# Kernel optimization log

Measured on AMD Instinct MI355X. Metric: run time of the kernel, lower is better.

Reference implementation:

```python
import jax, jax.numpy as jnp
import numpy as np

NEG_SLOPE = 0.2  # PyG GATConv default leaky_relu negative_slope
BN_EPS = 1e-5


def gat_layer(x, src, dst, W, a_src, a_dst, bias):
    """PyG-style GATConv (self-loops already appended to src/dst).
    x: [N, F_in], W: [F_in, H*C], a_src/a_dst: [H, C], bias: [H*C].
    Returns [N, H*C] (concat heads)."""
    N = x.shape[0]
    H, C = a_src.shape
    h = (x @ W).reshape(N, H, C)                      # [N, H, C]
    al_src = jnp.sum(h * a_src[None], axis=-1)        # [N, H]
    al_dst = jnp.sum(h * a_dst[None], axis=-1)        # [N, H]
    e = jax.nn.leaky_relu(al_src[src] + al_dst[dst], NEG_SLOPE)  # [E, H]
    # segment softmax over destination neighborhoods
    m = jax.ops.segment_max(e, dst, num_segments=N)   # [N, H]
    ee = jnp.exp(e - m[dst])
    denom = jax.ops.segment_sum(ee, dst, num_segments=N)  # [N, H]
    alpha = ee / denom[dst]                           # [E, H]
    out = jax.ops.segment_sum(alpha[:, :, None] * h[src], dst, num_segments=N)  # [N, H, C]
    return out.reshape(N, H * C) + bias


def batch_norm(x, gamma, beta):
    mu = jnp.mean(x, axis=0)
    var = jnp.var(x, axis=0)  # biased, matches torch BN training stats
    return gamma * (x - mu) * jax.lax.rsqrt(var + BN_EPS) + beta


def setup_inputs() -> dict:
    key = jax.random.key(0)
    N, F, H, C = 50000, 128, 4, 64
    E = 400000
    HC = H * C  # 256
    ks = jax.random.split(key, 24)

    def glorot(k, shape, fan_in):
        return jax.random.normal(k, shape, dtype=jnp.float32) * (1.0 / np.sqrt(fan_in))

    inp = {
        "x": jax.random.normal(ks[0], (N, F), dtype=jnp.float32),
        "edge_index": jax.random.randint(ks[1], (2, E), 0, N, dtype=jnp.int64),
        # conv1: F -> H*C
        "W1": glorot(ks[2], (F, HC), F),
        "a1s": glorot(ks[3], (H, C), C),
        "a1d": glorot(ks[4], (H, C), C),
        "b1": jnp.zeros((HC,), jnp.float32),
        # conv2: H*C -> H*C
        "W2": glorot(ks[5], (HC, HC), HC),
        "a2s": glorot(ks[6], (H, C), C),
        "a2d": glorot(ks[7], (H, C), C),
        "b2": jnp.zeros((HC,), jnp.float32),
        # conv3: H*C -> C (1 head)
        "W3": glorot(ks[8], (HC, C), HC),
        "a3s": glorot(ks[9], (1, C), C),
        "a3d": glorot(ks[10], (1, C), C),
        "b3": jnp.zeros((C,), jnp.float32),
        # batch norms
        "g1": jnp.ones((HC,), jnp.float32),
        "be1": jnp.zeros((HC,), jnp.float32),
        "g2": jnp.ones((HC,), jnp.float32),
        "be2": jnp.zeros((HC,), jnp.float32),
        # MLP head: C -> C//2 -> 2
        "fw1": glorot(ks[11], (C, C // 2), C),
        "fb1": jnp.zeros((C // 2,), jnp.float32),
        "fw2": glorot(ks[12], (C // 2, 2), C // 2),
        "fb2": jnp.zeros((2,), jnp.float32),
    }
    return inp


def reference(x, edge_index, W1, a1s, a1d, b1, W2, a2s, a2d, b2,
              W3, a3s, a3d, b3, g1, be1, g2, be2, fw1, fb1, fw2, fb2):
    N = x.shape[0]
    loop = jnp.arange(N, dtype=edge_index.dtype)
    src = jnp.concatenate([edge_index[0], loop])  # self-loops (PyG default)
    dst = jnp.concatenate([edge_index[1], loop])

    h = gat_layer(x, src, dst, W1, a1s, a1d, b1)
    h = jax.nn.elu(batch_norm(h, g1, be1))
    h = gat_layer(h, src, dst, W2, a2s, a2d, b2)
    h = jax.nn.elu(batch_norm(h, g2, be2))
    h = jax.nn.elu(gat_layer(h, src, dst, W3, a3s, a3d, b3))
    h = jax.nn.relu(h @ fw1 + fb1)
    return h @ fw2 + fb2  # [N, 2] logits
```

## Files before the change

### kernel.cpp

```cpp
#include <hip/hip_runtime.h>
#include <math.h>
#include <stdint.h>

typedef __attribute__((ext_vector_type(8))) short short8v;
typedef __attribute__((ext_vector_type(4))) float float4v;

__device__ __forceinline__ float bf2f(unsigned short u) {
  return __uint_as_float((unsigned int)u << 16);
}
__device__ __forceinline__ unsigned short f2bf(float f) {
  unsigned int u = __float_as_uint(f);
  unsigned int r = (u + 0x7FFFu + ((u >> 16) & 1u)) >> 16;
  return (unsigned short)r;
}
__device__ __forceinline__ float exp_lrelu(float x) {
  x = x > 0.f ? x : 0.2f * x;
  return expf(x);
}

typedef __attribute__((address_space(3))) void lds_void;
typedef const __attribute__((address_space(1))) void glb_void;
__device__ __forceinline__ void gload_lds16(const void* g, void* l) {
  __builtin_amdgcn_global_load_lds((glb_void*)g, (lds_void*)l, 16, 0, 0);
}

__device__ __forceinline__ void wprep_one(const float* W, unsigned short* Wh,
                                          int t, int K, int Nw)
{
  int i = t & 7;
  int lane = (t >> 3) & 63;
  int frag = t >> 9;
  int ktiles = K >> 5;
  int n_tile = frag / ktiles, k_tile = frag - n_tile * ktiles;
  int k = k_tile * 32 + ((lane >> 4) << 3) + i;
  int n = (n_tile << 4) + (lane & 15);
  Wh[t] = f2bf(W[(size_t)k * Nw + n]);
}

__global__ void wprep_all_kernel(const float* __restrict__ W1, unsigned short* __restrict__ w1h,
                                 const float* __restrict__ W2, unsigned short* __restrict__ w2h,
                                 const float* __restrict__ W3, unsigned short* __restrict__ w3h)
{
  int t = blockIdx.x * 256 + threadIdx.x;
  const int s1 = 128 * 256, s2 = 256 * 256, s3 = 256 * 64;
  if (t < s1) { wprep_one(W1, w1h, t, 128, 256); return; }
  t -= s1;
  if (t < s2) { wprep_one(W2, w2h, t, 256, 256); return; }
  t -= s2;
  if (t < s3) { wprep_one(W3, w3h, t, 256, 64); }
}

__global__ __launch_bounds__(256) void split_kernel(const float* __restrict__ in,
    unsigned short* __restrict__ hi, size_t n4)
{
  size_t i0 = (size_t)blockIdx.x * 256 + threadIdx.x;
  size_t stride = (size_t)gridDim.x * 256;
  for (size_t idx = i0; idx < n4; idx += stride) {
    float4 v = ((const float4*)in)[idx];
    ushort4 h;
    h.x = f2bf(v.x); h.y = f2bf(v.y); h.z = f2bf(v.z); h.w = f2bf(v.w);
    ((ushort4*)hi)[idx] = h;
  }
}

__global__ __launch_bounds__(256) void bnsplit_kernel(const unsigned short* __restrict__ act,
    const float* __restrict__ scale, const float* __restrict__ shift,
    unsigned short* __restrict__ hi, size_t nchunks)
{
  size_t i0 = (size_t)blockIdx.x * 256 + threadIdx.x;
  size_t stride = (size_t)gridDim.x * 256;
  for (size_t idx = i0; idx < nchunks; idx += stride) {
    ushort4 u = ((const ushort4*)act)[idx];
    int f = (int)((idx * 4) & 255);
    float4 sc = *(const float4*)(scale + f);
    float4 sh = *(const float4*)(shift + f);
    float v0 = fmaf(bf2f(u.x), sc.x, sh.x);
    float v1 = fmaf(bf2f(u.y), sc.y, sh.y);
    float v2 = fmaf(bf2f(u.z), sc.z, sh.z);
    float v3 = fmaf(bf2f(u.w), sc.w, sh.w);
    v0 = v0 > 0.f ? v0 : expm1f(v0);
    v1 = v1 > 0.f ? v1 : expm1f(v1);
    v2 = v2 > 0.f ? v2 : expm1f(v2);
    v3 = v3 > 0.f ? v3 : expm1f(v3);
    ushort4 h;
    h.x = f2bf(v0); h.y = f2bf(v1); h.z = f2bf(v2); h.w = f2bf(v3);
    ((ushort4*)hi)[idx] = h;
  }
}

template<int MI, int WM, int WN, int KSTEPS, int HEADS>
__global__ __launch_bounds__(128) void gemm_al(
    const unsigned short* __restrict__ Ah, const unsigned short* __restrict__ Bh,
    const float* __restrict__ a_s, const float* __restrict__ a_d,
    unsigned short* __restrict__ C, float* __restrict__ al_s, float* __restrict__ al_d,
    int M)
{
  constexpr int NWAVES = WM * WN;
  constexpr int BM = WM * MI * 16;
  constexpr int TILEB = BM * 64 * 2;
  constexpr int Nw = HEADS * 64;
  constexpr int K = KSTEPS * 64;
  constexpr int KT32 = KSTEPS * 2;
  __shared__ __align__(16) unsigned char smem[2][TILEB];

  const int wid = threadIdx.x >> 6, lane = threadIdx.x & 63;
  const int wm = wid / WN, wn = wid % WN;
  const int gn = blockIdx.y * WN + wn;
  const int m0 = blockIdx.x * BM;
  const int n0 = gn * 64;
  const int ar = lane & 15;
  const int cchunk = lane >> 4;
  const int ntile0 = n0 >> 4;

  float4v acc[MI][4];
#pragma unroll
  for (int mi = 0; mi < MI; ++mi)
#pragma unroll
    for (int ni = 0; ni < 4; ++ni)
      acc[mi][ni] = (float4v){0.f, 0.f, 0.f, 0.f};

  auto stage = [&](int buf, int ks) {
#pragma unroll
    for (int c = wid; c < 8; c += NWAVES) {
      const unsigned short* gp = Ah + (size_t)(m0 + lane) * K + ks * 64 + c * 8;
      gload_lds16(gp, &smem[buf][c * 1024 + lane * 16]);
    }
  };

  stage(0, 0);
  int cur = 0;
  for (int ks = 0; ks < KSTEPS; ++ks) {
    __syncthreads();
    short8v bh[2][4];
#pragma unroll
    for (int hh = 0; hh < 2; ++hh)
#pragma unroll
      for (int ni = 0; ni < 4; ++ni) {
        int kt = ks * 2 + hh;
        size_t off = (((size_t)(ntile0 + ni) * KT32 + kt) * 64 + lane) * 8;
        bh[hh][ni] = *(const short8v*)(Bh + off);
      }
    if (ks + 1 < KSTEPS) stage(cur ^ 1, ks + 1);
    short8v ah[2][MI];
#pragma unroll
    for (int hh = 0; hh < 2; ++hh)
#pragma unroll
      for (int mi = 0; mi < MI; ++mi) {
        int row = wm * MI * 16 + mi * 16 + ar;
        int c = hh * 4 + cchunk;
        int off = c * 1024 + row * 16;
        ah[hh][mi] = *(const short8v*)&smem[cur][off];
      }
#pragma unroll
    for (int hh = 0; hh < 2; ++hh)
#pragma unroll
      for (int mi = 0; mi < MI; ++mi)
#pragma unroll
        for (int ni = 0; ni < 4; ++ni)
          acc[mi][ni] = __builtin_amdgcn_mfma_f32_16x16x32_bf16(ah[hh][mi], bh[hh][ni], acc[mi][ni], 0, 0, 0);
    cur ^= 1;
  }

  const int cc = lane & 15;
#pragma unroll
  for (int mi = 0; mi < MI; ++mi) {
    int rowb = m0 + wm * MI * 16 + mi * 16 + ((lane >> 4) << 2);
#pragma unroll
    for (int r = 0; r < 4; ++r) {
      int row = rowb + r;
      if (row < M) {
#pragma unroll
        for (int ni = 0; ni < 4; ++ni)
          C[(size_t)row * Nw + n0 + ni * 16 + cc] = f2bf(acc[mi][ni][r]);
      }
    }
  }

  const int head = (HEADS == 4) ? gn : 0;
  float as_[4], ad_[4];
#pragma unroll
  for (int ni = 0; ni < 4; ++ni) {
    as_[ni] = a_s[head * 64 + ni * 16 + cc];
    ad_[ni] = a_d[head * 64 + ni * 16 + cc];
  }
#pragma unroll
  for (int mi = 0; mi < MI; ++mi) {
#pragma unroll
    for (int r = 0; r < 4; ++r) {
      float h0 = bf2f(f2bf(acc[mi][0][r]));
      float h1 = bf2f(f2bf(acc[mi][1][r]));
      float h2 = bf2f(f2bf(acc[mi][2][r]));
      float h3 = bf2f(f2bf(acc[mi][3][r]));
      float ps = h0 * as_[0] + h1 * as_[1] + h2 * as_[2] + h3 * as_[3];
      float pd = h0 * ad_[0] + h1 * ad_[1] + h2 * ad_[2] + h3 * ad_[3];
#pragma unroll
      for (int off = 1; off < 16; off <<= 1) {
        ps += __shfl_xor(ps, off);
        pd += __shfl_xor(pd, off);
      }
      int row = m0 + wm * MI * 16 + mi * 16 + ((lane >> 4) << 2) + r;
      if (cc == 0 && row < M) {
        al_s[row * HEADS + head] = ps;
        al_d[row * HEADS + head] = pd;
      }
    }
  }
}

__global__ void count_kernel(const int* __restrict__ dst, int E, int Etot, int* __restrict__ counts)
{
  int e = blockIdx.x * 256 + threadIdx.x;
  if (e >= Etot) return;
  int d = (e < E) ? dst[e] : (e - E);
  atomicAdd(&counts[d], 1);
}

__global__ void block_sum_kernel(const int* __restrict__ counts, int N, int* __restrict__ bsums)
{
  __shared__ int sd[256];
  int i = blockIdx.x * 256 + threadIdx.x;
  sd[threadIdx.x] = (i < N) ? counts[i] : 0;
  __syncthreads();
  for (int off = 128; off; off >>= 1) {
    if (threadIdx.x < off) sd[threadIdx.x] += sd[threadIdx.x + off];
    __syncthreads();
  }
  if (threadIdx.x == 0) bsums[blockIdx.x] = sd[0];
}

__global__ void scan_bsums_kernel(int* bsums, int nb)
{
  __shared__ int sd[256];
  int t = threadIdx.x;
  int v = (t < nb) ? bsums[t] : 0;
  sd[t] = v;
  __syncthreads();
  for (int off = 1; off < 256; off <<= 1) {
    int x = (t >= off) ? sd[t - off] : 0;
    __syncthreads();
    sd[t] += x;
    __syncthreads();
  }
  if (t < nb) bsums[t] = sd[t] - v;
}

__global__ void scan_write_kernel(const int* __restrict__ counts, int N,
                                  const int* __restrict__ bsums, int* __restrict__ rowStart, int Etot)
{
  __shared__ int sd[256];
  int i = blockIdx.x * 256 + threadIdx.x;
  int v = (i < N) ? counts[i] : 0;
  sd[threadIdx.x] = v;
  __syncthreads();
  for (int off = 1; off < 256; off <<= 1) {
    int x = (threadIdx.x >= off) ? sd[threadIdx.x - off] : 0;
    __syncthreads();
    sd[threadIdx.x] += x;
    __syncthreads();
  }
  if (i < N) rowStart[i] = bsums[blockIdx.x] + sd[threadIdx.x] - v;
  if (i == N - 1) rowStart[N] = Etot;
}

__global__ void fill_kernel(const int* __restrict__ src, const int* __restrict__ dst,
                            int E, int Etot, const int* __restrict__ rowStart,
                            int* __restrict__ cursor, int* __restrict__ csrSrc)
{
  int e = blockIdx.x * 256 + threadIdx.x;
  if (e >= Etot) return;
  int s, d;
  if (e < E) { s = src[e]; d = dst[e]; } else { s = d = e - E; }
  int pos = rowStart[d] + atomicAdd(&cursor[d], 1);
  csrSrc[pos] = s;
}

template<int HC_, bool OUT16>
__global__ __launch_bounds__(256) void aggregate_fused(
    const unsigned short* __restrict__ h16,
    const float* __restrict__ als, const float* __restrict__ ald,
    const int* __restrict__ csrSrc, const int* __restrict__ rowStart,
    void* __restrict__ outp, int N, const float* __restrict__ bias, int doElu)
{
  constexpr int H_ = HC_ / 64;
  constexpr int FPL = HC_ / 64;
  __shared__ float ldsW[4][64 * H_];
  const int wl = threadIdx.x >> 6;
  int wid = blockIdx.x * 4 + wl;
  if (wid >= N) return;
  const int lane = threadIdx.x & 63;
  const int head = (H_ == 4) ? (lane >> 4) : 0;
  const int start = rowStart[wid], end = rowStart[wid + 1];

  float ad0, ad1, ad2, ad3;
  if (H_ == 4) {
    float4 adv = ((const float4*)ald)[wid];
    ad0 = adv.x; ad1 = adv.y; ad2 = adv.z; ad3 = adv.w;
  } else {
    ad0 = ald[wid]; ad1 = ad2 = ad3 = 0.f;
  }

  float acc[FPL] = {};
  float wsum = 0.f;

  for (int base = start; base < end; base += 64) {
    int cnt = end - base; if (cnt > 64) cnt = 64;
    int s_l = 0;
    if (lane < cnt) {
      s_l = csrSrc[base + lane];
      if (H_ == 4) {
        float4 av = ((const float4*)als)[s_l];
        float4 w4;
        w4.x = exp_lrelu(av.x + ad0);
        w4.y = exp_lrelu(av.y + ad1);
        w4.z = exp_lrelu(av.z + ad2);
        w4.w = exp_lrelu(av.w + ad3);
        *(float4*)&ldsW[wl][lane * 4] = w4;
      } else {
        ldsW[wl][lane] = exp_lrelu(als[s_l] + ad0);
      }
    }
    int i = 0;
    for (; i + 4 <= cnt; i += 4) {
      int s0 = __shfl(s_l, i);
      int s1 = __shfl(s_l, i + 1);
      int s2 = __shfl(s_l, i + 2);
      int s3 = __shfl(s_l, i + 3);
      float w0 = ldsW[wl][(i + 0) * H_ + head];
      float w1 = ldsW[wl][(i + 1) * H_ + head];
      float w2 = ldsW[wl][(i + 2) * H_ + head];
      float w3 = ldsW[wl][(i + 3) * H_ + head];
      if (FPL == 4) {
        ushort4 r0 = ((const ushort4*)(h16 + (size_t)s0 * HC_))[lane];
        ushort4 r1 = ((const ushort4*)(h16 + (size_t)s1 * HC_))[lane];
        ushort4 r2 = ((const ushort4*)(h16 + (size_t)s2 * HC_))[lane];
        ushort4 r3 = ((const ushort4*)(h16 + (size_t)s3 * HC_))[lane];
        wsum += (w0 + w1) + (w2 + w3);
        acc[0] = fmaf(w0, bf2f(r0.x), acc[0]);
        acc[1] = fmaf(w0, bf2f(r0.y), acc[1]);
        acc[2] = fmaf(w0, bf2f(r0.z), acc[2]);
        acc[3] = fmaf(w0, bf2f(r0.w), acc[3]);
        acc[0] = fmaf(w1, bf2f(r1.x), acc[0]);
        acc[1] = fmaf(w1, bf2f(r1.y), acc[1]);
        acc[2] = fmaf(w1, bf2f(r1.z), acc[2]);
        acc[3] = fmaf(w1, bf2f(r1.w), acc[3]);
        acc[0] = fmaf(w2, bf2f(r2.x), acc[0]);
        acc[1] = fmaf(w2, bf2f(r2.y), acc[1]);
        acc[2] = fmaf(w2, bf2f(r2.z), acc[2]);
        acc[3] = fmaf(w2, bf2f(r2.w), acc[3]);
        acc[0] = fmaf(w3, bf2f(r3.x), acc[0]);
        acc[1] = fmaf(w3, bf2f(r3.y), acc[1]);
        acc[2] = fmaf(w3, bf2f(r3.z), acc[2]);
        acc[3] = fmaf(w3, bf2f(r3.w), acc[3]);
      } else {
        unsigned short r0 = h16[(size_t)s0 * HC_ + lane];
        unsigned short r1 = h16[(size_t)s1 * HC_ + lane];
        unsigned short r2 = h16[(size_t)s2 * HC_ + lane];
        unsigned short r3 = h16[(size_t)s3 * HC_ + lane];
        wsum += (w0 + w1) + (w2 + w3);
        acc[0] = fmaf(w0, bf2f(r0), acc[0]);
        acc[0] = fmaf(w1, bf2f(r1), acc[0]);
        acc[0] = fmaf(w2, bf2f(r2), acc[0]);
        acc[0] = fmaf(w3, bf2f(r3), acc[0]);
      }
    }
    for (; i < cnt; ++i) {
      int s0 = __shfl(s_l, i);
      float w0 = ldsW[wl][i * H_ + head];
      wsum += w0;
      if (FPL == 4) {
        ushort4 r0 = ((const ushort4*)(h16 + (size_t)s0 * HC_))[lane];
        acc[0] = fmaf(w0, bf2f(r0.x), acc[0]);
        acc[1] = fmaf(w0, bf2f(r0.y), acc[1]);
        acc[2] = fmaf(w0, bf2f(r0.z), acc[2]);
        acc[3] = fmaf(w0, bf2f(r0.w), acc[3]);
      } else {
        unsigned short r0 = h16[(size_t)s0 * HC_ + lane];
        acc[0] = fmaf(w0, bf2f(r0), acc[0]);
      }
    }
  }

  float inv = 1.0f / wsum;
  if (FPL == 4) {
    float o0 = acc[0] * inv, o1 = acc[1] * inv, o2 = acc[2] * inv, o3 = acc[3] * inv;
    if (bias) {
      const float4 b = ((const float4*)bias)[lane];
      o0 += b.x; o1 += b.y; o2 += b.z; o3 += b.w;
    }
    if (doElu) {
      o0 = o0 > 0.f ? o0 : expm1f(o0);
      o1 = o1 > 0.f ? o1 : expm1f(o1);
      o2 = o2 > 0.f ? o2 : expm1f(o2);
      o3 = o3 > 0.f ? o3 : expm1f(o3);
    }
    if (OUT16) {
      ushort4 o;
      o.x = f2bf(o0); o.y = f2bf(o1); o.z = f2bf(o2); o.w = f2bf(o3);
      ((ushort4*)((unsigned short*)outp + (size_t)wid * HC_))[lane] = o;
    } else {
      ((float4*)((float*)outp + (size_t)wid * HC_))[lane] = make_float4(o0, o1, o2, o3);
    }
  } else {
    float o = acc[0] * inv;
    if (bias) o += bias[lane];
    if (doElu) o = o > 0.f ? o : expm1f(o);
    if (OUT16) ((unsigned short*)outp)[(size_t)wid * HC_ + lane] = f2bf(o);
    else       ((float*)outp)[(size_t)wid * HC_ + lane] = o;
  }
}

__global__ __launch_bounds__(256) void bn_stats_kernel(const unsigned short* __restrict__ x, int N,
                                float* __restrict__ partials)
{
  const int wid = threadIdx.x >> 6, lane = threadIdx.x & 63;
  const int gw = blockIdx.x * 4 + wid;
  const int tw = gridDim.x * 4;
  float4 s = make_float4(0.f, 0.f, 0.f, 0.f);
  float4 q = make_float4(0.f, 0.f, 0.f, 0.f);
#pragma unroll 4
  for (int r = gw; r < N; r += tw) {
    ushort4 u = ((const ushort4*)(x + (size_t)r * 256))[lane];
    float v0 = bf2f(u.x), v1 = bf2f(u.y), v2 = bf2f(u.z), v3 = bf2f(u.w);
    s.x += v0; s.y += v1; s.z += v2; s.w += v3;
    q.x = fmaf(v0, v0, q.x); q.y = fmaf(v1, v1, q.y);
    q.z = fmaf(v2, v2, q.z); q.w = fmaf(v3, v3, q.w);
  }
  __shared__ float ls[4][512];
  *(float4*)&ls[wid][lane * 4] = s;
  *(float4*)&ls[wid][256 + lane * 4] = q;
  __syncthreads();
  const int t = threadIdx.x;
  float a = ls[0][t] + ls[1][t] + ls[2][t] + ls[3][t];
  float b = ls[0][t + 256] + ls[1][t + 256] + ls[2][t + 256] + ls[3][t + 256];
  partials[blockIdx.x * 512 + t] = a;
  partials[blockIdx.x * 512 + 256 + t] = b;
}

__global__ void bn_final_kernel(const float* __restrict__ partials, int nblk,
                                const float* __restrict__ g, const float* __restrict__ be,
                                int N, float* __restrict__ scale, float* __restrict__ shift)
{
  int f = threadIdx.x;
  float s = 0.f, q = 0.f;
#pragma unroll 8
  for (int b = 0; b < nblk; ++b) {
    s += partials[b * 512 + f];
    q += partials[b * 512 + 256 + f];
  }
  float mu = s / N;
  float var = q / N - mu * mu;
  float rs = rsqrtf(var + 1e-5f);
  float sc = g[f] * rs;
  scale[f] = sc;
  shift[f] = be[f] - mu * sc;
}

__global__ __launch_bounds__(256) void mlp_kernel(const float* __restrict__ h,
                           const float* __restrict__ fw1,
                           const float* __restrict__ fb1, const float* __restrict__ fw2,
                           const float* __restrict__ fb2, float* __restrict__ out, int N)
{
  __shared__ float w1s[64][32];
  __shared__ float w2s[32][2];
  __shared__ float b1s[32];
  const int t = threadIdx.x;
  for (int i = t; i < 64 * 32; i += 256) w1s[i >> 5][i & 31] = fw1[i];
  if (t < 64) w2s[t >> 1][t & 1] = fw2[t];
  if (t < 32) b1s[t] = fb1[t];
  __syncthreads();

  int n = blockIdx.x * 256 + t;
  if (n >= N) return;

  float hv[64];
#pragma unroll
  for (int k4 = 0; k4 < 16; ++k4) {
    float4 v = *(const float4*)(h + (size_t)n * 64 + k4 * 4);
    hv[k4 * 4 + 0] = v.x; hv[k4 * 4 + 1] = v.y;
    hv[k4 * 4 + 2] = v.z; hv[k4 * 4 + 3] = v.w;
  }
  float hid[32];
#pragma unroll
  for (int j = 0; j < 32; ++j) hid[j] = b1s[j];
#pragma unroll
  for (int k = 0; k < 64; ++k) {
    float hk = hv[k];
#pragma unroll
    for (int jb = 0; jb < 8; ++jb) {
      float4 wv = *(const float4*)&w1s[k][jb * 4];
      hid[jb * 4 + 0] = fmaf(hk, wv.x, hid[jb * 4 + 0]);
      hid[jb * 4 + 1] = fmaf(hk, wv.y, hid[jb * 4 + 1]);
      hid[jb * 4 + 2] = fmaf(hk, wv.z, hid[jb * 4 + 2]);
      hid[jb * 4 + 3] = fmaf(hk, wv.w, hid[jb * 4 + 3]);
    }
  }
  float p0 = fb2[0], p1 = fb2[1];
#pragma unroll
  for (int j = 0; j < 32; ++j) {
    float r = fmaxf(hid[j], 0.f);
    p0 = fmaf(r, w2s[j][0], p0);
    p1 = fmaf(r, w2s[j][1], p1);
  }
  *(float2*)(out + (size_t)n * 2) = make_float2(p0, p1);
}

extern "C" void kernel_launch(void* const* d_in, const int* in_sizes, int n_in,
                              void* d_out, int out_size, void* d_ws, size_t ws_size,
                              hipStream_t stream)
{
  const float* x   = (const float*)d_in[0];
  const int*   ei  = (const int*)d_in[1];
  const float* W1  = (const float*)d_in[2];
  const float* a1s = (const float*)d_in[3];
  const float* a1d = (const float*)d_in[4];
  const float* W2  = (const float*)d_in[6];
  const float* a2s = (const float*)d_in[7];
  const float* a2d = (const float*)d_in[8];
  const float* W3  = (const float*)d_in[10];
  const float* a3s = (const float*)d_in[11];
  const float* a3d = (const float*)d_in[12];
  const float* b3  = (const float*)d_in[13];
  const float* g1  = (const float*)d_in[14];
  const float* be1 = (const float*)d_in[15];
  const float* g2  = (const float*)d_in[16];
  const float* be2 = (const float*)d_in[17];
  const float* fw1 = (const float*)d_in[18];
  const float* fb1 = (const float*)d_in[19];
  const float* fw2 = (const float*)d_in[20];
  const float* fb2 = (const float*)d_in[21];
  float* out = (float*)d_out;

  const int F = 128;
  const int N = in_sizes[0] / F;
  const int E = in_sizes[1] / 2;
  const int Etot = E + N;
  const int* srcIdx = ei;
  const int* dstIdx = ei + E;

  char* w = (char*)d_ws;
  auto alloc = [&](size_t bytes) -> void* {
    void* p = (void*)w;
    w += (bytes + 255) & ~(size_t)255;
    return p;
  };
  unsigned short* h16  = (unsigned short*)alloc((size_t)N * 256 * 2);
  unsigned short* act16= (unsigned short*)alloc((size_t)N * 256 * 2);
  float* actf    = (float*)alloc((size_t)N * 64 * 4);
  unsigned short* aBf  = (unsigned short*)alloc((size_t)N * 256 * 2);
  float* als     = (float*)alloc((size_t)N * 4 * 4);
  float* ald     = (float*)alloc((size_t)N * 4 * 4);
  const size_t cntPad = ((size_t)N * 4 + 255) & ~(size_t)255;
  int*   counts  = (int*)alloc((size_t)N * 4);
  int*   cursor  = (int*)alloc((size_t)N * 4);
  int*   rowStart= (int*)alloc((size_t)(N + 1) * 4);
  int*   csrSrc  = (int*)alloc((size_t)Etot * 4);
  int*   bsums   = (int*)alloc((size_t)((N + 255) / 256) * 4);
  float* partials= (float*)alloc((size_t)128 * 512 * 4);
  float* scale1  = (float*)alloc(256 * 4);
  float* shift1  = (float*)alloc(256 * 4);
  float* scale2  = (float*)alloc(256 * 4);
  float* shift2  = (float*)alloc(256 * 4);
  unsigned short* w1h = (unsigned short*)alloc((size_t)128 * 256 * 2);
  unsigned short* w2h = (unsigned short*)alloc((size_t)256 * 256 * 2);
  unsigned short* w3h = (unsigned short*)alloc((size_t)256 * 64 * 2);
  (void)alloc(65536);

  const int nb = (N + 255) / 256;
  const int ebk = (Etot + 255) / 256;
  const int aggBlocks = (N + 3) / 4;

  const int wtot = 128 * 256 + 256 * 256 + 256 * 64;
  wprep_all_kernel<<<(wtot + 255) / 256, 256, 0, stream>>>(W1, w1h, W2, w2h, W3, w3h);

  hipMemsetAsync(counts, 0, cntPad + (size_t)N * 4, stream);
  count_kernel<<<ebk, 256, 0, stream>>>(dstIdx, E, Etot, counts);
  block_sum_kernel<<<nb, 256, 0, stream>>>(counts, N, bsums);
  scan_bsums_kernel<<<1, 256, 0, stream>>>(bsums, nb);
  scan_write_kernel<<<nb, 256, 0, stream>>>(counts, N, bsums, rowStart, Etot);
  fill_kernel<<<ebk, 256, 0, stream>>>(srcIdx, dstIdx, E, Etot, rowStart, cursor, csrSrc);

  dim3 g12((N + 63) / 64, 2);
  dim3 g3((N + 63) / 64, 1);

  split_kernel<<<2048, 256, 0, stream>>>(x, aBf, (size_t)N * 128 / 4);
  gemm_al<4, 1, 2, 2, 4><<<g12, 128, 0, stream>>>(aBf, w1h, a1s, a1d, h16, als, ald, N);
  aggregate_fused<256, true><<<aggBlocks, 256, 0, stream>>>(h16, als, ald, csrSrc, rowStart, act16, N, nullptr, 0);
  bn_stats_kernel<<<128, 256, 0, stream>>>(act16, N, partials);
  bn_final_kernel<<<1, 256, 0, stream>>>(partials, 128, g1, be1, N, scale1, shift1);

  bnsplit_kernel<<<2048, 256, 0, stream>>>(act16, scale1, shift1, aBf, (size_t)N * 64);
  gemm_al<4, 1, 2, 4, 4><<<g12, 128, 0, stream>>>(aBf, w2h, a2s, a2d, h16, als, ald, N);
  aggregate_fused<256, true><<<aggBlocks, 256, 0, stream>>>(h16, als, ald, csrSrc, rowStart, act16, N, nullptr, 0);
  bn_stats_kernel<<<128, 256, 0, stream>>>(act16, N, partials);
  bn_final_kernel<<<1, 256, 0, stream>>>(partials, 128, g2, be2, N, scale2, shift2);

  bnsplit_kernel<<<2048, 256, 0, stream>>>(act16, scale2, shift2, aBf, (size_t)N * 64);
  gemm_al<2, 2, 1, 4, 1><<<g3, 128, 0, stream>>>(aBf, w3h, a3s, a3d, h16, als, ald, N);
  aggregate_fused<64, false><<<aggBlocks, 256, 0, stream>>>(h16, als, ald, csrSrc, rowStart, actf, N, b3, 1);

  mlp_kernel<<<(N + 255) / 256, 256, 0, stream>>>(actf, fw1, fb1, fw2, fb2, out, N);
}
```

Measured before the change: 306.1 us.

## Fuse bf16 conversion and BN+ELU into GEMM A-loads, fuse MLP into last aggregation

Removes the standalone split and bnsplit kernels by loading the fp32 input or the bf16 activations directly in the GEMM, applying the BN scale/shift and ELU in registers, and writing the result to LDS. The global_load_lds staging is replaced by register loads followed by an LDS write after the MFMAs, which keeps double buffering. The layer-3 aggregation now also runs the MLP head per node, dropping the fp32 intermediate buffer and the separate mlp kernel. This saves several full-tensor memory round trips and launches. In exchange, the GEMM repeats the expm1 work for each N-tile block and does more VALU work and register traffic per tile.

```diff
diff --git a/kernel.cpp b/kernel.cpp
--- a/kernel.cpp
+++ b/kernel.cpp
@@ -16,12 +16,6 @@
 __device__ __forceinline__ float exp_lrelu(float x) {
   x = x > 0.f ? x : 0.2f * x;
   return expf(x);
-}
-
-typedef __attribute__((address_space(3))) void lds_void;
-typedef const __attribute__((address_space(1))) void glb_void;
-__device__ __forceinline__ void gload_lds16(const void* g, void* l) {
-  __builtin_amdgcn_global_load_lds((glb_void*)g, (lds_void*)l, 16, 0, 0);
 }
 
 __device__ __forceinline__ void wprep_one(const float* W, unsigned short* Wh,
@@ -50,60 +44,23 @@
   if (t < s3) { wprep_one(W3, w3h, t, 256, 64); }
 }
 
-__global__ __launch_bounds__(256) void split_kernel(const float* __restrict__ in,
-    unsigned short* __restrict__ hi, size_t n4)
-{
-  size_t i0 = (size_t)blockIdx.x * 256 + threadIdx.x;
-  size_t stride = (size_t)gridDim.x * 256;
-  for (size_t idx = i0; idx < n4; idx += stride) {
-    float4 v = ((const float4*)in)[idx];
-    ushort4 h;
-    h.x = f2bf(v.x); h.y = f2bf(v.y); h.z = f2bf(v.z); h.w = f2bf(v.w);
-    ((ushort4*)hi)[idx] = h;
-  }
-}
-
-__global__ __launch_bounds__(256) void bnsplit_kernel(const unsigned short* __restrict__ act,
+template<int MI, int WM, int WN, int KSTEPS, int HEADS, bool SRCF32>
+__global__ __launch_bounds__(128) void gemm_bn_al(
+    const void* __restrict__ AsrcV,
     const float* __restrict__ scale, const float* __restrict__ shift,
-    unsigned short* __restrict__ hi, size_t nchunks)
-{
-  size_t i0 = (size_t)blockIdx.x * 256 + threadIdx.x;
-  size_t stride = (size_t)gridDim.x * 256;
-  for (size_t idx = i0; idx < nchunks; idx += stride) {
-    ushort4 u = ((const ushort4*)act)[idx];
-    int f = (int)((idx * 4) & 255);
-    float4 sc = *(const float4*)(scale + f);
-    float4 sh = *(const float4*)(shift + f);
-    float v0 = fmaf(bf2f(u.x), sc.x, sh.x);
-    float v1 = fmaf(bf2f(u.y), sc.y, sh.y);
-    float v2 = fmaf(bf2f(u.z), sc.z, sh.z);
-    float v3 = fmaf(bf2f(u.w), sc.w, sh.w);
-    v0 = v0 > 0.f ? v0 : expm1f(v0);
-    v1 = v1 > 0.f ? v1 : expm1f(v1);
-    v2 = v2 > 0.f ? v2 : expm1f(v2);
-    v3 = v3 > 0.f ? v3 : expm1f(v3);
-    ushort4 h;
-    h.x = f2bf(v0); h.y = f2bf(v1); h.z = f2bf(v2); h.w = f2bf(v3);
-    ((ushort4*)hi)[idx] = h;
-  }
-}
-
-template<int MI, int WM, int WN, int KSTEPS, int HEADS>
-__global__ __launch_bounds__(128) void gemm_al(
-    const unsigned short* __restrict__ Ah, const unsigned short* __restrict__ Bh,
+    const unsigned short* __restrict__ Bh,
     const float* __restrict__ a_s, const float* __restrict__ a_d,
     unsigned short* __restrict__ C, float* __restrict__ al_s, float* __restrict__ al_d,
     int M)
 {
-  constexpr int NWAVES = WM * WN;
   constexpr int BM = WM * MI * 16;
-  constexpr int TILEB = BM * 64 * 2;
   constexpr int Nw = HEADS * 64;
   constexpr int K = KSTEPS * 64;
   constexpr int KT32 = KSTEPS * 2;
-  __shared__ __align__(16) unsigned char smem[2][TILEB];
-
-  const int wid = threadIdx.x >> 6, lane = threadIdx.x & 63;
+  __shared__ __align__(16) unsigned char smem[2][8192];
+
+  const int tid = threadIdx.x;
+  const int wid = tid >> 6, lane = tid & 63;
   const int wm = wid / WN, wn = wid % WN;
   const int gn = blockIdx.y * WN + wn;
   const int m0 = blockIdx.x * BM;
@@ -111,6 +68,7 @@
   const int ar = lane & 15;
   const int cchunk = lane >> 4;
   const int ntile0 = n0 >> 4;
+  const int srow = min(m0 + (tid & 63), M - 1);
 
   float4v acc[MI][4];
 #pragma unroll
@@ -119,15 +77,53 @@
     for (int ni = 0; ni < 4; ++ni)
       acc[mi][ni] = (float4v){0.f, 0.f, 0.f, 0.f};
 
-  auto stage = [&](int buf, int ks) {
-#pragma unroll
-    for (int c = wid; c < 8; c += NWAVES) {
-      const unsigned short* gp = Ah + (size_t)(m0 + lane) * K + ks * 64 + c * 8;
-      gload_lds16(gp, &smem[buf][c * 1024 + lane * 16]);
+  float4 rv0[4], rv1[4];
+  short8v ru[4];
+
+  auto LOADS = [&](int ks) {
+#pragma unroll
+    for (int j = 0; j < 4; ++j) {
+      int c = 2 * j + wid;
+      if constexpr (SRCF32) {
+        const float* p = (const float*)AsrcV + (size_t)srow * K + ks * 64 + c * 8;
+        rv0[j] = *(const float4*)p;
+        rv1[j] = *(const float4*)(p + 4);
+      } else {
+        const unsigned short* p = (const unsigned short*)AsrcV + (size_t)srow * K + ks * 64 + c * 8;
+        ru[j] = *(const short8v*)p;
+      }
     }
   };
-
-  stage(0, 0);
+  auto XWRITE = [&](int buf, int ks) {
+#pragma unroll
+    for (int j = 0; j < 4; ++j) {
+      int c = 2 * j + wid;
+      int r = tid & 63;
+      short8v wv;
+      if constexpr (SRCF32) {
+        float v[8] = {rv0[j].x, rv0[j].y, rv0[j].z, rv0[j].w,
+                      rv1[j].x, rv1[j].y, rv1[j].z, rv1[j].w};
+#pragma unroll
+        for (int i = 0; i < 8; ++i) wv[i] = (short)f2bf(v[i]);
+      } else {
+        int f = ks * 64 + c * 8;
+        float4 sc0 = *(const float4*)(scale + f), sc1 = *(const float4*)(scale + f + 4);
+        float4 sh0 = *(const float4*)(shift + f), sh1 = *(const float4*)(shift + f + 4);
+        float sc[8] = {sc0.x, sc0.y, sc0.z, sc0.w, sc1.x, sc1.y, sc1.z, sc1.w};
+        float sh[8] = {sh0.x, sh0.y, sh0.z, sh0.w, sh1.x, sh1.y, sh1.z, sh1.w};
+#pragma unroll
+        for (int i = 0; i < 8; ++i) {
+          float t = fmaf(bf2f((unsigned short)ru[j][i]), sc[i], sh[i]);
+          t = t > 0.f ? t : expm1f(t);
+          wv[i] = (short)f2bf(t);
+        }
+      }
+      *(short8v*)&smem[buf][c * 1024 + r * 16] = wv;
+    }
+  };
+
+  LOADS(0);
+  XWRITE(0, 0);
   int cur = 0;
   for (int ks = 0; ks < KSTEPS; ++ks) {
     __syncthreads();
@@ -140,7 +136,7 @@
         size_t off = (((size_t)(ntile0 + ni) * KT32 + kt) * 64 + lane) * 8;
         bh[hh][ni] = *(const short8v*)(Bh + off);
       }
-    if (ks + 1 < KSTEPS) stage(cur ^ 1, ks + 1);
+    if (ks + 1 < KSTEPS) LOADS(ks + 1);
     short8v ah[2][MI];
 #pragma unroll
     for (int hh = 0; hh < 2; ++hh)
@@ -148,8 +144,7 @@
       for (int mi = 0; mi < MI; ++mi) {
         int row = wm * MI * 16 + mi * 16 + ar;
         int c = hh * 4 + cchunk;
-        int off = c * 1024 + row * 16;
-        ah[hh][mi] = *(const short8v*)&smem[cur][off];
+        ah[hh][mi] = *(const short8v*)&smem[cur][c * 1024 + row * 16];
       }
 #pragma unroll
     for (int hh = 0; hh < 2; ++hh)
@@ -158,6 +153,7 @@
 #pragma unroll
         for (int ni = 0; ni < 4; ++ni)
           acc[mi][ni] = __builtin_amdgcn_mfma_f32_16x16x32_bf16(ah[hh][mi], bh[hh][ni], acc[mi][ni], 0, 0, 0);
+    if (ks + 1 < KSTEPS) XWRITE(cur ^ 1, ks + 1);
     cur ^= 1;
   }
 
@@ -274,32 +270,22 @@
   csrSrc[pos] = s;
 }
 
-template<int HC_, bool OUT16>
-__global__ __launch_bounds__(256) void aggregate_fused(
+__global__ __launch_bounds__(256) void aggregate_fused4(
     const unsigned short* __restrict__ h16,
     const float* __restrict__ als, const float* __restrict__ ald,
     const int* __restrict__ csrSrc, const int* __restrict__ rowStart,
-    void* __restrict__ outp, int N, const float* __restrict__ bias, int doElu)
-{
-  constexpr int H_ = HC_ / 64;
-  constexpr int FPL = HC_ / 64;
-  __shared__ float ldsW[4][64 * H_];
+    unsigned short* __restrict__ outp, int N)
+{
+  __shared__ float ldsW[4][256];
   const int wl = threadIdx.x >> 6;
   int wid = blockIdx.x * 4 + wl;
   if (wid >= N) return;
   const int lane = threadIdx.x & 63;
-  const int head = (H_ == 4) ? (lane >> 4) : 0;
+  const int head = lane >> 4;
   const int start = rowStart[wid], end = rowStart[wid + 1];
 
-  float ad0, ad1, ad2, ad3;
-  if (H_ == 4) {
-    float4 adv = ((const float4*)ald)[wid];
-    ad0 = adv.x; ad1 = adv.y; ad2 = adv.z; ad3 = adv.w;
-  } else {
-    ad0 = ald[wid]; ad1 = ad2 = ad3 = 0.f;
-  }
-
-  float acc[FPL] = {};
+  float4 adv = ((const float4*)ald)[wid];
+  float acc[4] = {};
   float wsum = 0.f;
 
   for (int base = start; base < end; base += 64) {
@@ -307,17 +293,13 @@
     int s_l = 0;
     if (lane < cnt) {
       s_l = csrSrc[base + lane];
-      if (H_ == 4) {
-        float4 av = ((const float4*)als)[s_l];
-        float4 w4;
-        w4.x = exp_lrelu(av.x + ad0);
-        w4.y = exp_lrelu(av.y + ad1);
-        w4.z = exp_lrelu(av.z + ad2);
-        w4.w = exp_lrelu(av.w + ad3);
-        *(float4*)&ldsW[wl][lane * 4] = w4;
-      } else {
-        ldsW[wl][lane] = exp_lrelu(als[s_l] + ad0);
-      }
+      float4 av = ((const float4*)als)[s_l];
+      float4 w4;
+      w4.x = exp_lrelu(av.x + adv.x);
+      w4.y = exp_lrelu(av.y + adv.y);
+      w4.z = exp_lrelu(av.z + adv.z);
+      w4.w = exp_lrelu(av.w + adv.w);
+      *(float4*)&ldsW[wl][lane * 4] = w4;
     }
     int i = 0;
     for (; i + 4 <= cnt; i += 4) {
@@ -325,88 +307,127 @@
       int s1 = __shfl(s_l, i + 1);
       int s2 = __shfl(s_l, i + 2);
       int s3 = __shfl(s_l, i + 3);
-      float w0 = ldsW[wl][(i + 0) * H_ + head];
-      float w1 = ldsW[wl][(i + 1) * H_ + head];
-      float w2 = ldsW[wl][(i + 2) * H_ + head];
-      float w3 = ldsW[wl][(i + 3) * H_ + head];
-      if (FPL == 4) {
-        ushort4 r0 = ((const ushort4*)(h16 + (size_t)s0 * HC_))[lane];
-        ushort4 r1 = ((const ushort4*)(h16 + (size_t)s1 * HC_))[lane];
-        ushort4 r2 = ((const ushort4*)(h16 + (size_t)s2 * HC_))[lane];
-        ushort4 r3 = ((const ushort4*)(h16 + (size_t)s3 * HC_))[lane];
-        wsum += (w0 + w1) + (w2 + w3);
-        acc[0] = fmaf(w0, bf2f(r0.x), acc[0]);
-        acc[1] = fmaf(w0, bf2f(r0.y), acc[1]);
-        acc[2] = fmaf(w0, bf2f(r0.z), acc[2]);
-        acc[3] = fmaf(w0, bf2f(r0.w), acc[3]);
-        acc[0] = fmaf(w1, bf2f(r1.x), acc[0]);
-        acc[1] = fmaf(w1, bf2f(r1.y), acc[1]);
-        acc[2] = fmaf(w1, bf2f(r1.z), acc[2]);
-        acc[3] = fmaf(w1, bf2f(r1.w), acc[3]);
-        acc[0] = fmaf(w2, bf2f(r2.x), acc[0]);
-        acc[1] = fmaf(w2, bf2f(r2.y), acc[1]);
-        acc[2] = fmaf(w2, bf2f(r2.z), acc[2]);
-        acc[3] = fmaf(w2, bf2f(r2.w), acc[3]);
-        acc[0] = fmaf(w3, bf2f(r3.x), acc[0]);
-        acc[1] = fmaf(w3, bf2f(r3.y), acc[1]);
-        acc[2] = fmaf(w3, bf2f(r3.z), acc[2]);
-        acc[3] = fmaf(w3, bf2f(r3.w), acc[3]);
-      } else {
-        unsigned short r0 = h16[(size_t)s0 * HC_ + lane];
-        unsigned short r1 = h16[(size_t)s1 * HC_ + lane];
-        unsigned short r2 = h16[(size_t)s2 * HC_ + lane];
-        unsigned short r3 = h16[(size_t)s3 * HC_ + lane];
-        wsum += (w0 + w1) + (w2 + w3);
-        acc[0] = fmaf(w0, bf2f(r0), acc[0]);
-        acc[0] = fmaf(w1, bf2f(r1), acc[0]);
-        acc[0] = fmaf(w2, bf2f(r2), acc[0]);
-        acc[0] = fmaf(w3, bf2f(r3), acc[0]);
-      }
+      float w0 = ldsW[wl][(i + 0) * 4 + head];
+      float w1 = ldsW[wl][(i + 1) * 4 + head];
+      float w2 = ldsW[wl][(i + 2) * 4 + head];
+      float w3 = ldsW[wl][(i + 3) * 4 + head];
+      ushort4 r0 = ((const ushort4*)(h16 + (size_t)s0 * 256))[lane];
+      ushort4 r1 = ((const ushort4*)(h16 + (size_t)s1 * 256))[lane];
+      ushort4 r2 = ((const ushort4*)(h16 + (size_t)s2 * 256))[lane];
+      ushort4 r3 = ((const ushort4*)(h16 + (size_t)s3 * 256))[lane];
+      wsum += (w0 + w1) + (w2 + w3);
+      acc[0] = fmaf(w0, bf2f(r0.x), acc[0]);
+      acc[1] = fmaf(w0, bf2f(r0.y), acc[1]);
+      acc[2] = fmaf(w0, bf2f(r0.z), acc[2]);
+      acc[3] = fmaf(w0, bf2f(r0.w), acc[3]);
+      acc[0] = fmaf(w1, bf2f(r1.x), acc[0]);
+      acc[1] = fmaf(w1, bf2f(r1.y), acc[1]);
+      acc[2] = fmaf(w1, bf2f(r1.z), acc[2]);
+      acc[3] = fmaf(w1, bf2f(r1.w), acc[3]);
+      acc[0] = fmaf(w2, bf2f(r2.x), acc[0]);
+      acc[1] = fmaf(w2, bf2f(r2.y), acc[1]);
+      acc[2] = fmaf(w2, bf2f(r2.z), acc[2]);
+      acc[3] = fmaf(w2, bf2f(r2.w), acc[3]);
+      acc[0] = fmaf(w3, bf2f(r3.x), acc[0]);
+      acc[1] = fmaf(w3, bf2f(r3.y), acc[1]);
+      acc[2] = fmaf(w3, bf2f(r3.z), acc[2]);
+      acc[3] = fmaf(w3, bf2f(r3.w), acc[3]);
     }
     for (; i < cnt; ++i) {
       int s0 = __shfl(s_l, i);
-      float w0 = ldsW[wl][i * H_ + head];
+      float w0 = ldsW[wl][i * 4 + head];
       wsum += w0;
-      if (FPL == 4) {
-        ushort4 r0 = ((const ushort4*)(h16 + (size_t)s0 * HC_))[lane];
-        acc[0] = fmaf(w0, bf2f(r0.x), acc[0]);
-        acc[1] = fmaf(w0, bf2f(r0.y), acc[1]);
-        acc[2] = fmaf(w0, bf2f(r0.z), acc[2]);
-        acc[3] = fmaf(w0, bf2f(r0.w), acc[3]);
-      } else {
-        unsigned short r0 = h16[(size_t)s0 * HC_ + lane];
-        acc[0] = fmaf(w0, bf2f(r0), acc[0]);
-      }
+      ushort4 r0 = ((const ushort4*)(h16 + (size_t)s0 * 256))[lane];
+      acc[0] = fmaf(w0, bf2f(r0.x), acc[0]);
+      acc[1] = fmaf(w0, bf2f(r0.y), acc[1]);
+      acc[2] = fmaf(w0, bf2f(r0.z), acc[2]);
+      acc[3] = fmaf(w0, bf2f(r0.w), acc[3]);
     }
   }
 
   float inv = 1.0f / wsum;
-  if (FPL == 4) {
-    float o0 = acc[0] * inv, o1 = acc[1] * inv, o2 = acc[2] * inv, o3 = acc[3] * inv;
-    if (bias) {
-      const float4 b = ((const float4*)bias)[lane];
-      o0 += b.x; o1 += b.y; o2 += b.z; o3 += b.w;
-    }
-    if (doElu) {
-      o0 = o0 > 0.f ? o0 : expm1f(o0);
-      o1 = o1 > 0.f ? o1 : expm1f(o1);
-      o2 = o2 > 0.f ? o2 : expm1f(o2);
-      o3 = o3 > 0.f ? o3 : expm1f(o3);
-    }
-    if (OUT16) {
-      ushort4 o;
-      o.x = f2bf(o0); o.y = f2bf(o1); o.z = f2bf(o2); o.w = f2bf(o3);
-      ((ushort4*)((unsigned short*)outp + (size_t)wid * HC_))[lane] = o;
-    } else {
-      ((float4*)((float*)outp + (size_t)wid * HC_))[lane] = make_float4(o0, o1, o2, o3);
-    }
-  } else {
-    float o = acc[0] * inv;
-    if (bias) o += bias[lane];
-    if (doElu) o = o > 0.f ? o : expm1f(o);
-    if (OUT16) ((unsigned short*)outp)[(size_t)wid * HC_ + lane] = f2bf(o);
-    else       ((float*)outp)[(size_t)wid * HC_ + lane] = o;
-  }
+  ushort4 o;
+  o.x = f2bf(acc[0] * inv); o.y = f2bf(acc[1] * inv);
+  o.z = f2bf(acc[2] * inv); o.w = f2bf(acc[3] * inv);
+  ((ushort4*)(outp + (size_t)wid * 256))[lane] = o;
+}
+
+__global__ __launch_bounds__(256) void agg3_mlp_kernel(
+    const unsigned short* __restrict__ h16,
+    const float* __restrict__ als, const float* __restrict__ ald,
+    const int* __restrict__ csrSrc, const int* __restrict__ rowStart,
+    const float* __restrict__ b3,
+    const float* __restrict__ fw1, const float* __restrict__ fb1,
+    const float* __restrict__ fw2, const float* __restrict__ fb2,
+    float* __restrict__ out, int N)
+{
+  __shared__ float ldsW[4][64];
+  __shared__ float w1s[64][32];
+  __shared__ float w2s[32][2];
+  __shared__ float b1s[32];
+  __shared__ float mrow[4][64];
+  const int t = threadIdx.x;
+  for (int i = t; i < 2048; i += 256) w1s[i >> 5][i & 31] = fw1[i];
+  if (t < 64) w2s[t >> 1][t & 1] = fw2[t];
+  if (t < 32) b1s[t] = fb1[t];
+  __syncthreads();
+
+  const int wl = t >> 6, lane = t & 63;
+  int wid = blockIdx.x * 4 + wl;
+  if (wid >= N) return;
+  const int start = rowStart[wid], end = rowStart[wid + 1];
+  const float ad0 = ald[wid];
+
+  float acc = 0.f, wsum = 0.f;
+  for (int base = start; base < end; base += 64) {
+    int cnt = end - base; if (cnt > 64) cnt = 64;
+    int s_l = 0;
+    if (lane < cnt) {
+      s_l = csrSrc[base + lane];
+      ldsW[wl][lane] = exp_lrelu(als[s_l] + ad0);
+    }
+    int i = 0;
+    for (; i + 4 <= cnt; i += 4) {
+      int s0 = __shfl(s_l, i);
+      int s1 = __shfl(s_l, i + 1);
+      int s2 = __shfl(s_l, i + 2);
+      int s3 = __shfl(s_l, i + 3);
+      float w0 = ldsW[wl][i + 0];
+      float w1 = ldsW[wl][i + 1];
+      float w2 = ldsW[wl][i + 2];
+      float w3 = ldsW[wl][i + 3];
+      unsigned short r0 = h16[(size_t)s0 * 64 + lane];
+      unsigned short r1 = h16[(size_t)s1 * 64 + lane];
+      unsigned short r2 = h16[(size_t)s2 * 64 + lane];
+      unsigned short r3 = h16[(size_t)s3 * 64 + lane];
+      wsum += (w0 + w1) + (w2 + w3);
+      acc = fmaf(w0, bf2f(r0), acc);
+      acc = fmaf(w1, bf2f(r1), acc);
+      acc = fmaf(w2, bf2f(r2), acc);
+      acc = fmaf(w3, bf2f(r3), acc);
+    }
+    for (; i < cnt; ++i) {
+      int s0 = __shfl(s_l, i);
+      float w0 = ldsW[wl][i];
+      wsum += w0;
+      unsigned short r0 = h16[(size_t)s0 * 64 + lane];
+      acc = fmaf(w0, bf2f(r0), acc);
+    }
+  }
+  float o = acc / wsum + b3[lane];
+  o = o > 0.f ? o : expm1f(o);
+
+  mrow[wl][lane] = o;
+  const int j = lane & 31, col = lane >> 5;
+  float hid = b1s[j];
+#pragma unroll
+  for (int k = 0; k < 64; ++k)
+    hid = fmaf(mrow[wl][k], w1s[k][j], hid);
+  hid = fmaxf(hid, 0.f);
+  float p = hid * w2s[j][col];
+#pragma unroll
+  for (int off = 1; off < 32; off <<= 1) p += __shfl_xor(p, off);
+  if (j == 0) out[(size_t)wid * 2 + col] = p + fb2[col];
 }
 
 __global__ __launch_bounds__(256) void bn_stats_kernel(const unsigned short* __restrict__ x, int N,
@@ -453,55 +474,6 @@
   float sc = g[f] * rs;
   scale[f] = sc;
   shift[f] = be[f] - mu * sc;
-}
-
-__global__ __launch_bounds__(256) void mlp_kernel(const float* __restrict__ h,
-                           const float* __restrict__ fw1,
-                           const float* __restrict__ fb1, const float* __restrict__ fw2,
-                           const float* __restrict__ fb2, float* __restrict__ out, int N)
-{
-  __shared__ float w1s[64][32];
-  __shared__ float w2s[32][2];
-  __shared__ float b1s[32];
-  const int t = threadIdx.x;
-  for (int i = t; i < 64 * 32; i += 256) w1s[i >> 5][i & 31] = fw1[i];
-  if (t < 64) w2s[t >> 1][t & 1] = fw2[t];
-  if (t < 32) b1s[t] = fb1[t];
-  __syncthreads();
-
-  int n = blockIdx.x * 256 + t;
-  if (n >= N) return;
-
-  float hv[64];
-#pragma unroll
-  for (int k4 = 0; k4 < 16; ++k4) {
-    float4 v = *(const float4*)(h + (size_t)n * 64 + k4 * 4);
-    hv[k4 * 4 + 0] = v.x; hv[k4 * 4 + 1] = v.y;
-    hv[k4 * 4 + 2] = v.z; hv[k4 * 4 + 3] = v.w;
-  }
-  float hid[32];
-#pragma unroll
-  for (int j = 0; j < 32; ++j) hid[j] = b1s[j];
-#pragma unroll
-  for (int k = 0; k < 64; ++k) {
-    float hk = hv[k];
-#pragma unroll
-    for (int jb = 0; jb < 8; ++jb) {
-      float4 wv = *(const float4*)&w1s[k][jb * 4];
-      hid[jb * 4 + 0] = fmaf(hk, wv.x, hid[jb * 4 + 0]);
-      hid[jb * 4 + 1] = fmaf(hk, wv.y, hid[jb * 4 + 1]);
-      hid[jb * 4 + 2] = fmaf(hk, wv.z, hid[jb * 4 + 2]);
-      hid[jb * 4 + 3] = fmaf(hk, wv.w, hid[jb * 4 + 3]);
-    }
-  }
-  float p0 = fb2[0], p1 = fb2[1];
-#pragma unroll
-  for (int j = 0; j < 32; ++j) {
-    float r = fmaxf(hid[j], 0.f);
-    p0 = fmaf(r, w2s[j][0], p0);
-    p1 = fmaf(r, w2s[j][1], p1);
-  }
-  *(float2*)(out + (size_t)n * 2) = make_float2(p0, p1);
 }
 
 extern "C" void kernel_launch(void* const* d_in, const int* in_sizes, int n_in,
@@ -545,8 +517,6 @@
   };
   unsigned short* h16  = (unsigned short*)alloc((size_t)N * 256 * 2);
   unsigned short* act16= (unsigned short*)alloc((size_t)N * 256 * 2);
-  float* actf    = (float*)alloc((size_t)N * 64 * 4);
-  unsigned short* aBf  = (unsigned short*)alloc((size_t)N * 256 * 2);
   float* als     = (float*)alloc((size_t)N * 4 * 4);
   float* ald     = (float*)alloc((size_t)N * 4 * 4);
   const size_t cntPad = ((size_t)N * 4 + 255) & ~(size_t)255;
@@ -582,21 +552,20 @@
   dim3 g12((N + 63) / 64, 2);
   dim3 g3((N + 63) / 64, 1);
 
-  split_kernel<<<2048, 256, 0, stream>>>(x, aBf, (size_t)N * 128 / 4);
-  gemm_al<4, 1, 2, 2, 4><<<g12, 128, 0, stream>>>(aBf, w1h, a1s, a1d, h16, als, ald, N);
-  aggregate_fused<256, true><<<aggBlocks, 256, 0, stream>>>(h16, als, ald, csrSrc, rowStart, act16, N, nullptr, 0);
+  gemm_bn_al<4, 1, 2, 2, 4, true><<<g12, 128, 0, stream>>>(
+      x, nullptr, nullptr, w1h, a1s, a1d, h16, als, ald, N);
+  aggregate_fused4<<<aggBlocks, 256, 0, stream>>>(h16, als, ald, csrSrc, rowStart, act16, N);
   bn_stats_kernel<<<128, 256, 0, stream>>>(act16, N, partials);
   bn_final_kernel<<<1, 256, 0, stream>>>(partials, 128, g1, be1, N, scale1, shift1);
 
-  bnsplit_kernel<<<2048, 256, 0, stream>>>(act16, scale1, shift1, aBf, (size_t)N * 64);
-  gemm_al<4, 1, 2, 4, 4><<<g12, 128, 0, stream>>>(aBf, w2h, a2s, a2d, h16, als, ald, N);
-  aggregate_fused<256, true><<<aggBlocks, 256, 0, stream>>>(h16, als, ald, csrSrc, rowStart, act16, N, nullptr, 0);
+  gemm_bn_al<4, 1, 2, 4, 4, false><<<g12, 128, 0, stream>>>(
+      act16, scale1, shift1, w2h, a2s, a2d, h16, als, ald, N);
+  aggregate_fused4<<<aggBlocks, 256, 0, stream>>>(h16, als, ald, csrSrc, rowStart, act16, N);
   bn_stats_kernel<<<128, 256, 0, stream>>>(act16, N, partials);
   bn_final_kernel<<<1, 256, 0, stream>>>(partials, 128, g2, be2, N, scale2, shift2);
 
-  bnsplit_kernel<<<2048, 256, 0, stream>>>(act16, scale2, shift2, aBf, (size_t)N * 64);
-  gemm_al<2, 2, 1, 4, 1><<<g3, 128, 0, stream>>>(aBf, w3h, a3s, a3d, h16, als, ald, N);
-  aggregate_fused<64, false><<<aggBlocks, 256, 0, stream>>>(h16, als, ald, csrSrc, rowStart, actf, N, b3, 1);
-
-  mlp_kernel<<<(N + 255) / 256, 256, 0, stream>>>(actf, fw1, fb1, fw2, fb2, out, N);
-}
+  gemm_bn_al<2, 2, 1, 4, 1, false><<<g3, 128, 0, stream>>>(
+      act16, scale2, shift2, w3h, a3s, a3d, h16, als, ald, N);
+  agg3_mlp_kernel<<<aggBlocks, 256, 0, stream>>>(h16, als, ald, csrSrc, rowStart,
+                                                 b3, fw1, fb1, fw2, fb2, out, N);
+}
```

Measured after the change: 314.9 us. 1.03x slower.
